# Kernel optimization log

Measured on AMD Instinct MI355X. Metric: run time of the kernel, lower is better.

## Reference

```python
import jax, jax.numpy as jnp
import numpy as np

WINDOW_SIZE = 11
SIGMA = 1.5
C1 = 0.01 ** 2
C2 = 0.03 ** 2


def _gaussian_window(channel, dtype):
    # 1D gaussian, normalized, then outer product -> 2D window [ws, ws]
    center = WINDOW_SIZE // 2
    x = jnp.arange(WINDOW_SIZE, dtype=jnp.float32) - center
    g = jnp.exp(-(x ** 2) / (2.0 * SIGMA ** 2))
    g = g / g.sum()
    w2d = jnp.outer(g, g)  # [ws, ws]
    # depthwise kernel: [C_out=channel, C_in/groups=1, ws, ws]
    return jnp.broadcast_to(w2d, (channel, 1, WINDOW_SIZE, WINDOW_SIZE)).astype(dtype)


def _depthwise_blur(x, window):
    pad = WINDOW_SIZE // 2
    return jax.lax.conv_general_dilated(
        x, window,
        window_strides=(1, 1),
        padding=[(pad, pad), (pad, pad)],
        feature_group_count=x.shape[1],
        dimension_numbers=('NCHW', 'OIHW', 'NCHW'))


def setup_inputs() -> dict:
    key = jax.random.key(0)
    k1, k2 = jax.random.split(key)
    img1 = jax.random.uniform(k1, (16, 3, 512, 512), dtype=jnp.float32)
    img2 = jax.random.uniform(k2, (16, 3, 512, 512), dtype=jnp.float32)
    return {"img1": img1, "img2": img2}


def reference(img1, img2):
    channel = img1.shape[1]
    window = _gaussian_window(channel, img1.dtype)

    mu1 = _depthwise_blur(img1, window)
    mu2 = _depthwise_blur(img2, window)
    mu1_sq = mu1 * mu1
    mu2_sq = mu2 * mu2
    mu1_mu2 = mu1 * mu2

    sigma1_sq = _depthwise_blur(img1 * img1, window) - mu1_sq
    sigma2_sq = _depthwise_blur(img2 * img2, window) - mu2_sq
    sigma12 = _depthwise_blur(img1 * img2, window) - mu1_mu2

    ssim_map = ((2.0 * mu1_mu2 + C1) * (2.0 * sigma12 + C2)) / (
        (mu1_sq + mu2_sq + C1) * (sigma1_sq + sigma2_sq + C2))
    return ssim_map.mean()  # size_average=True
```

## Files before the change

### kernel.cpp

```cpp
#include <hip/hip_runtime.h>


typedef _Float16 f16;
typedef __attribute__((ext_vector_type(8))) _Float16 f16x8;
typedef __attribute__((ext_vector_type(4))) float f32x4;

#define IMGW 512
#define IMGH 512
#define NPL 48
#define NBLOCKS (NPL * 8 * 8)
#define NPIX 12582912.0
#define REDT 1024

#define SRW 84
#define PR 74
#define IMGOFFD (PR * SRW)

#define INV_T 0.99967202f

__device__ const float G_dev[11] = {0.00102838f, 0.00759876f, 0.03600077f,
                                    0.10936069f, 0.21300554f, 0.26601172f,
                                    0.21300554f, 0.10936069f, 0.03600077f,
                                    0.00759876f, 0.00102838f};

__global__ __launch_bounds__(256, 3) void ssim_main(const float* __restrict__ img1,
                                                    const float* __restrict__ img2,
                                                    float* __restrict__ partial) {
    __shared__ __align__(16) float sP[2 * IMGOFFD];
    __shared__ float wsum[4];

    const int tid  = threadIdx.x;
    const int lane = tid & 63;
    const int wv   = tid >> 6;
    const int l15  = lane & 15;
    const int lg   = lane >> 4;

    const int bid   = blockIdx.x;
    const int plane = bid >> 6;
    const int rem   = bid & 63;
    const int by    = rem >> 3;
    const int bx    = rem & 7;
    const int R0    = by * 64 - 5;
    const int AC0   = bx * 64 - 8;

    const float* __restrict__ p1 = img1 + (size_t)plane * (IMGH * IMGW);
    const float* __restrict__ p2 = img2 + (size_t)plane * (IMGH * IMGW);

    const bool interior = (by >= 1) & (by <= 6) & (bx >= 1) & (bx <= 6);

    if (interior) {
        for (int r = wv; r < PR; r += 4) {
            if (lane < 21) {
                const float* gp = p1 + (size_t)(R0 + r) * IMGW + (AC0 + 4 * lane);
                __builtin_amdgcn_global_load_lds(gp, &sP[r * SRW], 16, 0, 0);
            }
        }
        for (int r = wv; r < PR; r += 4) {
            if (lane < 21) {
                const float* gp = p2 + (size_t)(R0 + r) * IMGW + (AC0 + 4 * lane);
                __builtin_amdgcn_global_load_lds(gp, &sP[IMGOFFD + r * SRW], 16, 0, 0);
            }
        }
    } else {
        for (int it = 0; it < 25; ++it) {
            const int i = tid + it * 256;
            if (i < IMGOFFD) ((float2*)sP)[i] = make_float2(0.0f, 0.0f);
        }
        __syncthreads();
        const int rlo = (R0 < 0) ? -R0 : 0;
        const int rhi = (R0 + PR > IMGH) ? (IMGH - R0) : PR;
        const int llo = (AC0 < 0) ? ((-AC0) >> 2) : 0;
        const int lhiT = (IMGW - AC0) >> 2;
        const int lhi = (lhiT < 21) ? lhiT : 21;
        for (int r = rlo + wv; r < rhi; r += 4) {
            if (lane >= llo && lane < lhi) {
                const float* gp = p1 + (size_t)(R0 + r) * IMGW + (AC0 + 4 * lane);
                __builtin_amdgcn_global_load_lds(gp, &sP[r * SRW], 16, 0, 0);
            }
        }
        for (int r = rlo + wv; r < rhi; r += 4) {
            if (lane >= llo && lane < lhi) {
                const float* gp = p2 + (size_t)(R0 + r) * IMGW + (AC0 + 4 * lane);
                __builtin_amdgcn_global_load_lds(gp, &sP[IMGOFFD + r * SRW], 16, 0, 0);
            }
        }
    }
    __syncthreads();

    f16x8 bbH, bbV;
    #pragma unroll
    for (int j = 0; j < 8; ++j) {
        const int kj = (j < 4) ? (4 * lg + j) : (16 + 4 * lg + (j - 4));
        const int tH = kj - l15 - 3;
        const int tV = kj - l15;
        bbH[j] = (f16)((tH >= 0 && tH < 11) ? G_dev[tH] : 0.0f);
        bbV[j] = (f16)((tV >= 0 && tV < 11) ? G_dev[tV] : 0.0f);
    }

    const f32x4 zero4 = {0.0f, 0.0f, 0.0f, 0.0f};

    const int rowA = 16 * wv + l15;
    int rowB = 16 * wv + 16 + l15;
    if (rowB > PR - 1) rowB = PR - 1;

    float acc = 0.0f;
    const float C1 = 1.0e-4f;
    const float C2 = 9.0e-4f;

    #pragma unroll
    for (int m = 0; m < 4; ++m) {
        const int cg = 16 * m + 4 * lg;
        f32x4 D0[5], D1[5];
        #pragma unroll
        for (int s = 0; s < 2; ++s) {
            const int row = s ? rowB : rowA;
            const float* __restrict__ r1 = &sP[row * SRW];
            const float* __restrict__ r2 = &sP[IMGOFFD + row * SRW];
            const f32x4 xa = *(const f32x4*)&r1[cg];
            const f32x4 xb = *(const f32x4*)&r1[cg + 16];
            const f32x4 ya = *(const f32x4*)&r2[cg];
            const f32x4 yb = *(const f32x4*)&r2[cg + 16];
            f16x8 fx, fy;
            #pragma unroll
            for (int e = 0; e < 4; ++e) {
                fx[e]     = (f16)xa[e];
                fx[e + 4] = (f16)xb[e];
                fy[e]     = (f16)ya[e];
                fy[e + 4] = (f16)yb[e];
            }
            const f16x8 fxx = fx * fx;
            const f16x8 fyy = fy * fy;
            const f16x8 fxy = fx * fy;
            f32x4* D = s ? D1 : D0;
            D[0] = __builtin_amdgcn_mfma_f32_16x16x32_f16(fx,  bbH, zero4, 0, 0, 0);
            D[1] = __builtin_amdgcn_mfma_f32_16x16x32_f16(fy,  bbH, zero4, 0, 0, 0);
            D[2] = __builtin_amdgcn_mfma_f32_16x16x32_f16(fxx, bbH, zero4, 0, 0, 0);
            D[3] = __builtin_amdgcn_mfma_f32_16x16x32_f16(fyy, bbH, zero4, 0, 0, 0);
            D[4] = __builtin_amdgcn_mfma_f32_16x16x32_f16(fxy, bbH, zero4, 0, 0, 0);
        }
        f32x4 h[5];
        #pragma unroll
        for (int q = 0; q < 5; ++q) {
            f16x8 av;
            #pragma unroll
            for (int j = 0; j < 4; ++j) {
                av[j]     = (f16)D0[q][j];
                av[j + 4] = (f16)D1[q][j];
            }
            h[q] = __builtin_amdgcn_mfma_f32_16x16x32_f16(av, bbV, zero4, 0, 0, 0);
            h[q] *= INV_T;
        }
        #pragma unroll
        for (int r = 0; r < 4; ++r) {
            const float mu1 = h[0][r], mu2 = h[1][r];
            const float exx = h[2][r], eyy = h[3][r], exy = h[4][r];
            const float mu1s = mu1 * mu1;
            const float mu2s = mu2 * mu2;
            const float mu12 = mu1 * mu2;
            const float s1  = exx - mu1s;
            const float s2  = eyy - mu2s;
            const float s12 = exy - mu12;
            const float num = fmaf(2.0f, mu12, C1) * fmaf(2.0f, s12, C2);
            const float den = (mu1s + mu2s + C1) * (s1 + s2 + C2);
            float rd = __builtin_amdgcn_rcpf(den);
            rd = rd * fmaf(-den, rd, 2.0f);
            acc = fmaf(num, rd, acc);
        }
    }

    #pragma unroll
    for (int off = 32; off > 0; off >>= 1)
        acc += __shfl_down(acc, off, 64);
    if (lane == 0) wsum[wv] = acc;
    __syncthreads();
    if (tid == 0)
        partial[bid] = (wsum[0] + wsum[1]) + (wsum[2] + wsum[3]);
}

__global__ __launch_bounds__(REDT) void ssim_reduce(const float* __restrict__ partial,
                                                    float* __restrict__ out) {
    const int tid = threadIdx.x;
    double s = 0.0;
    for (int i = tid; i < NBLOCKS; i += REDT)
        s += (double)partial[i];
    #pragma unroll
    for (int off = 32; off > 0; off >>= 1)
        s += __shfl_down(s, off, 64);
    __shared__ double wsd[REDT / 64];
    if ((tid & 63) == 0) wsd[tid >> 6] = s;
    __syncthreads();
    if (tid == 0) {
        double t = 0.0;
        #pragma unroll
        for (int i = 0; i < REDT / 64; ++i) t += wsd[i];
        out[0] = (float)(t / NPIX);
    }
}

extern "C" void kernel_launch(void* const* d_in, const int* in_sizes, int n_in,
                              void* d_out, int out_size, void* d_ws, size_t ws_size,
                              hipStream_t stream) {
    const float* img1 = (const float*)d_in[0];
    const float* img2 = (const float*)d_in[1];
    float* partial = (float*)d_ws;
    float* out = (float*)d_out;
    ssim_main<<<NBLOCKS, 256, 0, stream>>>(img1, img2, partial);
    ssim_reduce<<<1, REDT, 0, stream>>>(partial, out);
}
```

Measured before the change: 52.16 us.

## Make each wave load its own halo rows and drop block barrier

Each wave now fills only the 32 rows of shared memory it later reads, instead of the block cooperatively loading all rows. Each load instruction covers three rows at once, using 63 lanes laid out to match the LDS row stride. The block-wide __syncthreads after the load becomes a per-wave vmcnt wait, so waves can start computing as soon as their own data arrives. The cost is that rows shared by neighbouring waves are fetched twice, which adds L2 and LDS-write traffic.

```diff
diff --git a/kernel.cpp b/kernel.cpp
--- a/kernel.cpp
+++ b/kernel.cpp
@@ -48,44 +48,56 @@
 
     const bool interior = (by >= 1) & (by <= 6) & (bx >= 1) & (bx <= 6);
 
+    const int sub_r = lane / 21;
+    const int cgl   = lane - 21 * sub_r;
+    const int rbeg  = 16 * wv;
+    const int rend  = (rbeg + 32 < PR) ? rbeg + 32 : PR;
+
     if (interior) {
-        for (int r = wv; r < PR; r += 4) {
-            if (lane < 21) {
-                const float* gp = p1 + (size_t)(R0 + r) * IMGW + (AC0 + 4 * lane);
-                __builtin_amdgcn_global_load_lds(gp, &sP[r * SRW], 16, 0, 0);
-            }
-        }
-        for (int r = wv; r < PR; r += 4) {
-            if (lane < 21) {
-                const float* gp = p2 + (size_t)(R0 + r) * IMGW + (AC0 + 4 * lane);
-                __builtin_amdgcn_global_load_lds(gp, &sP[IMGOFFD + r * SRW], 16, 0, 0);
+        for (int rr = rbeg; rr < rend; rr += 3) {
+            const int row = rr + sub_r;
+            if (lane < 63 && row < rend) {
+                const float* gp = p1 + (size_t)(R0 + row) * IMGW + (AC0 + 4 * cgl);
+                __builtin_amdgcn_global_load_lds(gp, &sP[rr * SRW], 16, 0, 0);
+            }
+        }
+        for (int rr = rbeg; rr < rend; rr += 3) {
+            const int row = rr + sub_r;
+            if (lane < 63 && row < rend) {
+                const float* gp = p2 + (size_t)(R0 + row) * IMGW + (AC0 + 4 * cgl);
+                __builtin_amdgcn_global_load_lds(gp, &sP[IMGOFFD + rr * SRW], 16, 0, 0);
             }
         }
     } else {
-        for (int it = 0; it < 25; ++it) {
-            const int i = tid + it * 256;
-            if (i < IMGOFFD) ((float2*)sP)[i] = make_float2(0.0f, 0.0f);
+        {
+            const int nz = (rend - rbeg) * (SRW / 2);
+            float2* z1 = (float2*)&sP[rbeg * SRW];
+            float2* z2 = (float2*)&sP[IMGOFFD + rbeg * SRW];
+            const float2 zz = make_float2(0.0f, 0.0f);
+            for (int i = lane; i < nz; i += 64) { z1[i] = zz; z2[i] = zz; }
         }
         __syncthreads();
         const int rlo = (R0 < 0) ? -R0 : 0;
         const int rhi = (R0 + PR > IMGH) ? (IMGH - R0) : PR;
-        const int llo = (AC0 < 0) ? ((-AC0) >> 2) : 0;
-        const int lhiT = (IMGW - AC0) >> 2;
-        const int lhi = (lhiT < 21) ? lhiT : 21;
-        for (int r = rlo + wv; r < rhi; r += 4) {
-            if (lane >= llo && lane < lhi) {
-                const float* gp = p1 + (size_t)(R0 + r) * IMGW + (AC0 + 4 * lane);
-                __builtin_amdgcn_global_load_lds(gp, &sP[r * SRW], 16, 0, 0);
-            }
-        }
-        for (int r = rlo + wv; r < rhi; r += 4) {
-            if (lane >= llo && lane < lhi) {
-                const float* gp = p2 + (size_t)(R0 + r) * IMGW + (AC0 + 4 * lane);
-                __builtin_amdgcn_global_load_lds(gp, &sP[IMGOFFD + r * SRW], 16, 0, 0);
-            }
-        }
-    }
-    __syncthreads();
+        const bool cok = ((unsigned)(AC0 + 4 * cgl) < (unsigned)IMGW);
+        for (int rr = rbeg; rr < rend; rr += 3) {
+            const int row = rr + sub_r;
+            if (lane < 63 && row < rend && row >= rlo && row < rhi && cok) {
+                const float* gp = p1 + (size_t)(R0 + row) * IMGW + (AC0 + 4 * cgl);
+                __builtin_amdgcn_global_load_lds(gp, &sP[rr * SRW], 16, 0, 0);
+            }
+        }
+        for (int rr = rbeg; rr < rend; rr += 3) {
+            const int row = rr + sub_r;
+            if (lane < 63 && row < rend && row >= rlo && row < rhi && cok) {
+                const float* gp = p2 + (size_t)(R0 + row) * IMGW + (AC0 + 4 * cgl);
+                __builtin_amdgcn_global_load_lds(gp, &sP[IMGOFFD + rr * SRW], 16, 0, 0);
+            }
+        }
+    }
+
+    asm volatile("s_waitcnt vmcnt(0)" ::: "memory");
+    __builtin_amdgcn_sched_barrier(0);
 
     f16x8 bbH, bbV;
     #pragma unroll
```

New measurement: 52.24 us. About the same (+0.2%).

## Halve row tile height, split column groups across waves, use packed f16 conversion

Applied to the files above, without the earlier changes.

Tiles shrink from 64x64 to 32 rows by 64 columns, which doubles the block count. Each pair of waves now shares a 16-row group and splits its columns instead of covering separate row bands. The interior global-to-LDS load packs three rows per wave instruction, zero-fill uses 16-byte stores, and occupancy hint rises to 5 blocks. Float-to-half conversion switches to packed round-toward-zero cvt_pkrtz, which changes rounding slightly. The cost is a larger vertical halo relative to useful rows (42 loaded rows per 32 output rows) in exchange for more parallelism and less LDS per block.

```diff
diff --git a/kernel.cpp b/kernel.cpp
--- a/kernel.cpp
+++ b/kernel.cpp
@@ -2,18 +2,19 @@
 
 
 typedef _Float16 f16;
+typedef __attribute__((ext_vector_type(2))) _Float16 f16x2;
 typedef __attribute__((ext_vector_type(8))) _Float16 f16x8;
 typedef __attribute__((ext_vector_type(4))) float f32x4;
 
 #define IMGW 512
 #define IMGH 512
 #define NPL 48
-#define NBLOCKS (NPL * 8 * 8)
+#define NBLOCKS (NPL * 8 * 16)
 #define NPIX 12582912.0
 #define REDT 1024
 
 #define SRW 84
-#define PR 74
+#define PR 42
 #define IMGOFFD (PR * SRW)
 
 #define INV_T 0.99967202f
@@ -23,7 +24,15 @@
                                     0.21300554f, 0.10936069f, 0.03600077f,
                                     0.00759876f, 0.00102838f};
 
-__global__ __launch_bounds__(256, 3) void ssim_main(const float* __restrict__ img1,
+__device__ __forceinline__ f16x8 pk8(const f32x4 a, const f32x4 b) {
+    const f16x2 p0 = __builtin_bit_cast(f16x2, __builtin_amdgcn_cvt_pkrtz(a[0], a[1]));
+    const f16x2 p1 = __builtin_bit_cast(f16x2, __builtin_amdgcn_cvt_pkrtz(a[2], a[3]));
+    const f16x2 p2 = __builtin_bit_cast(f16x2, __builtin_amdgcn_cvt_pkrtz(b[0], b[1]));
+    const f16x2 p3 = __builtin_bit_cast(f16x2, __builtin_amdgcn_cvt_pkrtz(b[2], b[3]));
+    return (f16x8){p0[0], p0[1], p1[0], p1[1], p2[0], p2[1], p3[0], p3[1]};
+}
+
+__global__ __launch_bounds__(256, 5) void ssim_main(const float* __restrict__ img1,
                                                     const float* __restrict__ img2,
                                                     float* __restrict__ partial) {
     __shared__ __align__(16) float sP[2 * IMGOFFD];
@@ -36,52 +45,56 @@
     const int lg   = lane >> 4;
 
     const int bid   = blockIdx.x;
-    const int plane = bid >> 6;
-    const int rem   = bid & 63;
-    const int by    = rem >> 3;
-    const int bx    = rem & 7;
-    const int R0    = by * 64 - 5;
-    const int AC0   = bx * 64 - 8;
+    const int plane = bid >> 7;
+    const int rem   = bid & 127;
+    const int tyi   = rem >> 3;
+    const int txi   = rem & 7;
+    const int R0    = tyi * 32 - 5;
+    const int AC0   = txi * 64 - 8;
 
     const float* __restrict__ p1 = img1 + (size_t)plane * (IMGH * IMGW);
     const float* __restrict__ p2 = img2 + (size_t)plane * (IMGH * IMGW);
 
-    const bool interior = (by >= 1) & (by <= 6) & (bx >= 1) & (bx <= 6);
+    const bool interior = (tyi >= 1) & (tyi <= 14) & (txi >= 1) & (txi <= 6);
 
     if (interior) {
-        for (int r = wv; r < PR; r += 4) {
-            if (lane < 21) {
-                const float* gp = p1 + (size_t)(R0 + r) * IMGW + (AC0 + 4 * lane);
-                __builtin_amdgcn_global_load_lds(gp, &sP[r * SRW], 16, 0, 0);
+        const int sub_r = lane / 21;
+        const int cgl   = lane - 21 * sub_r;
+        #pragma unroll
+        for (int img = 0; img < 2; ++img) {
+            const float* __restrict__ bp = img ? p2 : p1;
+            float* lb = &sP[img * IMGOFFD];
+            for (int i = wv; i < 14; i += 4) {
+                const int rr = 3 * i;
+                if (lane < 63) {
+                    const float* gp = bp + (size_t)(R0 + rr + sub_r) * IMGW
+                                         + (AC0 + 4 * cgl);
+                    __builtin_amdgcn_global_load_lds(gp, &lb[rr * SRW], 16, 0, 0);
+                }
             }
         }
-        for (int r = wv; r < PR; r += 4) {
-            if (lane < 21) {
-                const float* gp = p2 + (size_t)(R0 + r) * IMGW + (AC0 + 4 * lane);
-                __builtin_amdgcn_global_load_lds(gp, &sP[IMGOFFD + r * SRW], 16, 0, 0);
-            }
-        }
     } else {
-        for (int it = 0; it < 25; ++it) {
+        const f32x4 zz = {0.0f, 0.0f, 0.0f, 0.0f};
+        #pragma unroll
+        for (int it = 0; it < 7; ++it) {
             const int i = tid + it * 256;
-            if (i < IMGOFFD) ((float2*)sP)[i] = make_float2(0.0f, 0.0f);
+            if (i < 2 * IMGOFFD / 4) ((f32x4*)sP)[i] = zz;
         }
         __syncthreads();
         const int rlo = (R0 < 0) ? -R0 : 0;
         const int rhi = (R0 + PR > IMGH) ? (IMGH - R0) : PR;
-        const int llo = (AC0 < 0) ? ((-AC0) >> 2) : 0;
-        const int lhiT = (IMGW - AC0) >> 2;
-        const int lhi = (lhiT < 21) ? lhiT : 21;
-        for (int r = rlo + wv; r < rhi; r += 4) {
-            if (lane >= llo && lane < lhi) {
-                const float* gp = p1 + (size_t)(R0 + r) * IMGW + (AC0 + 4 * lane);
-                __builtin_amdgcn_global_load_lds(gp, &sP[r * SRW], 16, 0, 0);
-            }
-        }
-        for (int r = rlo + wv; r < rhi; r += 4) {
-            if (lane >= llo && lane < lhi) {
-                const float* gp = p2 + (size_t)(R0 + r) * IMGW + (AC0 + 4 * lane);
-                __builtin_amdgcn_global_load_lds(gp, &sP[IMGOFFD + r * SRW], 16, 0, 0);
+        const bool cok = (lane < 21) &&
+                         ((unsigned)(AC0 + 4 * lane) < (unsigned)IMGW);
+        #pragma unroll
+        for (int img = 0; img < 2; ++img) {
+            const float* __restrict__ bp = img ? p2 : p1;
+            float* lb = &sP[img * IMGOFFD];
+            for (int r = rlo + wv; r < rhi; r += 4) {
+                if (cok) {
+                    const float* gp = bp + (size_t)(R0 + r) * IMGW
+                                         + (AC0 + 4 * lane);
+                    __builtin_amdgcn_global_load_lds(gp, &lb[r * SRW], 16, 0, 0);
+                }
             }
         }
     }
@@ -99,8 +112,10 @@
 
     const f32x4 zero4 = {0.0f, 0.0f, 0.0f, 0.0f};
 
-    const int rowA = 16 * wv + l15;
-    int rowB = 16 * wv + 16 + l15;
+    const int rg = wv >> 1;
+    const int ch = wv & 1;
+    const int rowA = 16 * rg + l15;
+    int rowB = rowA + 16;
     if (rowB > PR - 1) rowB = PR - 1;
 
     float acc = 0.0f;
@@ -108,8 +123,8 @@
     const float C2 = 9.0e-4f;
 
     #pragma unroll
-    for (int m = 0; m < 4; ++m) {
-        const int cg = 16 * m + 4 * lg;
+    for (int m = 0; m < 2; ++m) {
+        const int cg = 16 * (2 * ch + m) + 4 * lg;
         f32x4 D0[5], D1[5];
         #pragma unroll
         for (int s = 0; s < 2; ++s) {
@@ -120,14 +135,8 @@
             const f32x4 xb = *(const f32x4*)&r1[cg + 16];
             const f32x4 ya = *(const f32x4*)&r2[cg];
             const f32x4 yb = *(const f32x4*)&r2[cg + 16];
-            f16x8 fx, fy;
-            #pragma unroll
-            for (int e = 0; e < 4; ++e) {
-                fx[e]     = (f16)xa[e];
-                fx[e + 4] = (f16)xb[e];
-                fy[e]     = (f16)ya[e];
-                fy[e + 4] = (f16)yb[e];
-            }
+            const f16x8 fx = pk8(xa, xb);
+            const f16x8 fy = pk8(ya, yb);
             const f16x8 fxx = fx * fx;
             const f16x8 fyy = fy * fy;
             const f16x8 fxy = fx * fy;
```

Result: no change. 52.32 us (+0.3%).
